# Performance work log

Measured on AMD Instinct MI355X. Metric: run time of the kernel, lower is better.

The kernel has to match this reference:

```python
import jax, jax.numpy as jnp
import numpy as np

QK_NOPE = 128
QK_ROPE = 64
V_DIM = 128
N_HEADS = 16
ROPE_BASE = 10000.0
RMS_EPS = 1e-6


def _rms_norm(x, w, eps=RMS_EPS):
    x = x.astype(jnp.float32)
    var = jnp.mean(x * x, axis=-1, keepdims=True)
    return w * x * jax.lax.rsqrt(var + eps)


def _rotate_half(x):
    x1, x2 = jnp.split(x, 2, axis=-1)
    return jnp.concatenate([-x2, x1], axis=-1)


def _rope_cos_sin(position_ids, dim=QK_ROPE, base=ROPE_BASE):
    # factor=1.0 YaRN collapses to plain RoPE with mscale=1
    inv_freq = 1.0 / (base ** (jnp.arange(0, dim, 2, dtype=jnp.float32) / dim))
    freqs = position_ids.astype(jnp.float32)[..., None] * inv_freq  # [B,S,dim/2]
    emb = jnp.concatenate([freqs, freqs], axis=-1)                  # [B,S,dim]
    return jnp.cos(emb), jnp.sin(emb)


def setup_inputs() -> dict:
    key = jax.random.key(0)
    ks = jax.random.split(key, 8)
    B, S, H = 1, 2048, 4096
    q_lora, kv_lora = 1536, 512
    q_head = QK_NOPE + QK_ROPE
    s = lambda k, shp, fan: jax.random.normal(k, shp, jnp.float32) * (fan ** -0.5)
    return {
        "hidden_states": jax.random.normal(ks[0], (B, S, H), jnp.float32),
        "position_ids": jnp.broadcast_to(jnp.arange(S, dtype=jnp.int64), (B, S)),
        "wq_a": s(ks[1], (q_lora, H), H),
        "q_a_norm_w": jnp.ones((q_lora,), jnp.float32),
        "wq_b": s(ks[2], (N_HEADS * q_head, q_lora), q_lora),
        "wkv_a": s(ks[3], (kv_lora + QK_ROPE, H), H),
        "kv_a_norm_w": jnp.ones((kv_lora,), jnp.float32),
        "wkv_b": s(ks[4], (N_HEADS * (QK_NOPE + V_DIM), kv_lora), kv_lora),
        "wo": s(ks[5], (H, N_HEADS * V_DIM), N_HEADS * V_DIM),
    }


def reference(hidden_states, position_ids, wq_a, q_a_norm_w, wq_b, wkv_a,
              kv_a_norm_w, wkv_b, wo):
    B, S, _ = hidden_states.shape
    kv_lora = kv_a_norm_w.shape[0]
    q_head = QK_NOPE + QK_ROPE
    softmax_scale = q_head ** -0.5  # mscale_all_dim=0 -> no yarn correction

    # Q low-rank path
    q_lat = _rms_norm(hidden_states @ wq_a.T, q_a_norm_w).astype(hidden_states.dtype)
    q = (q_lat @ wq_b.T).reshape(B, S, N_HEADS, q_head)
    q_nope, q_pe = q[..., :QK_NOPE], q[..., QK_NOPE:]

    # KV low-rank path
    kv = hidden_states @ wkv_a.T
    compressed_kv = _rms_norm(kv[..., :kv_lora], kv_a_norm_w).astype(hidden_states.dtype)
    k_pe = kv[..., kv_lora:].reshape(B, S, 1, QK_ROPE)

    cos, sin = _rope_cos_sin(position_ids)
    cos_h, sin_h = cos[:, :, None, :], sin[:, :, None, :]
    q_pe = q_pe * cos_h + _rotate_half(q_pe) * sin_h
    k_pe = k_pe * cos_h + _rotate_half(k_pe) * sin_h

    kv_exp = (compressed_kv @ wkv_b.T).reshape(B, S, N_HEADS, QK_NOPE + V_DIM)
    k_nope, v = kv_exp[..., :QK_NOPE], kv_exp[..., QK_NOPE:]

    qf = jnp.concatenate([q_nope, q_pe], axis=-1).astype(jnp.float32)   # [B,S,H,Dq]
    kf = jnp.concatenate([k_nope, jnp.broadcast_to(k_pe, (B, S, N_HEADS, QK_ROPE))],
                         axis=-1).astype(jnp.float32)
    vf = v.astype(jnp.float32)

    scores = jnp.einsum('bqhd,bkhd->bhqk', qf, kf) * softmax_scale
    causal = jnp.tril(jnp.ones((S, S), dtype=bool))
    scores = jnp.where(causal, scores, -jnp.inf)
    probs = jax.nn.softmax(scores, axis=-1)
    out = jnp.einsum('bhqk,bkhd->bqhd', probs, vf).astype(hidden_states.dtype)
    out = out.reshape(B, S, N_HEADS * V_DIM)
    return out @ wo.T
```

## Files before the change

kernel.cpp:

```cpp
#include <hip/hip_runtime.h>
#include <hip/hip_bf16.h>


typedef short bf16x8 __attribute__((ext_vector_type(8)));
typedef float f32x4  __attribute__((ext_vector_type(4)));

#if __has_builtin(__builtin_amdgcn_global_load_lds)
#define USE_GLL 1
#else
#define USE_GLL 0
#endif

__device__ __forceinline__ void stage16(const void* g, void* l) {
#if USE_GLL
    __builtin_amdgcn_global_load_lds(
        (__attribute__((address_space(1))) void*)(g),
        (__attribute__((address_space(3))) void*)(l), 16, 0, 0);
#else
    *(uint4*)l = *(const uint4*)g;
#endif
}

#define LOG2E 1.4426950408889634f

__device__ __forceinline__ short bf16_bits(float v) {
    union { __hip_bfloat16 h; short s; } u;
    u.h = __float2bfloat16(v);
    return u.s;
}

__global__ __launch_bounds__(256)
void cvt_bf16(const float* __restrict__ s, __hip_bfloat16* __restrict__ d, int nq) {
    int i = blockIdx.x * 256 + threadIdx.x;
    if (i >= nq) return;
    float4 v = ((const float4*)s)[i];
    union { uint2 u; __hip_bfloat16 h[4]; } r;
    r.h[0] = __float2bfloat16(v.x); r.h[1] = __float2bfloat16(v.y);
    r.h[2] = __float2bfloat16(v.z); r.h[3] = __float2bfloat16(v.w);
    ((uint2*)d)[i] = r.u;
}

__global__ __launch_bounds__(256)
void zero_f32(float* __restrict__ p, int n4) {
    int i = blockIdx.x * 256 + threadIdx.x;
    if (i < n4) ((float4*)p)[i] = float4{0.f, 0.f, 0.f, 0.f};
}

__global__ __launch_bounds__(256)
void zero_u4(uint4* __restrict__ p, int n) {
    int i = blockIdx.x * 256 + threadIdx.x;
    if (i < n) p[i] = make_uint4(0u, 0u, 0u, 0u);
}

__global__ __launch_bounds__(256)
void kpe_copy(const float* __restrict__ fused, float* __restrict__ kpe) {
    int i = blockIdx.x * 256 + threadIdx.x;
    int r = i >> 6, c = i & 63;
    kpe[i] = fused[(size_t)r * 2112 + 2048 + c];
}

template<int OUTMODE>
__global__ __launch_bounds__(256)
void gemm_lds(const __hip_bfloat16* __restrict__ A,
              const __hip_bfloat16* __restrict__ B,
              void* __restrict__ C,
              int K, int Cld, int Nlim, int ksteps) {
    __shared__ __align__(16) short As[128 * 64];
    __shared__ __align__(16) short Bs[128 * 64];

    const int tid  = threadIdx.x;
    const int lane = tid & 63;
    const int wave = tid >> 6;
    const int quad = lane >> 4;
    const int l16  = lane & 15;

    const int gx = gridDim.x, gy = gridDim.y;
    const int nwg = gx * gy * gridDim.z;
    const int f   = blockIdx.x + gx * (blockIdx.y + gy * blockIdx.z);
    const int qc  = nwg >> 3, rc = nwg & 7;
    const int xcd = f & 7, idx = f >> 3;
    const int neu = (xcd < rc ? xcd * (qc + 1) : rc * (qc + 1) + (xcd - rc) * qc) + idx;
    const int bx  = neu % gx;
    const int t1  = neu / gx;
    const int by  = t1 % gy;
    const int bz  = t1 / gy;

    const int m0 = by * 128;
    const int n0 = bx * 128;
    const int wm = (wave >> 1) * 64;
    const int wn = (wave & 1) * 64;
    const int kbeg = bz * ksteps * 64;

    const int lrow = lane >> 3;
    const int lchk = lane & 7;
    const int sb   = (lchk ^ lrow) * 16;

    f32x4 acc[4][4];
    #pragma unroll
    for (int i = 0; i < 4; i++)
        #pragma unroll
        for (int j = 0; j < 4; j++)
            acc[i][j] = f32x4{0.f, 0.f, 0.f, 0.f};

    const size_t str = (size_t)K * 2;
    const char* Ab = (const char*)A;
    const char* Bb = (const char*)B;

    for (int kk = 0; kk < ksteps; kk++) {
        if (kk) __syncthreads();
        const size_t koff = (size_t)(kbeg + kk * 64) * 2;
        #pragma unroll
        for (int t = 0; t < 4; t++) {
            const int row = wave * 32 + t * 8 + lrow;
            stage16(Ab + (size_t)(m0 + row) * str + koff + sb,
                    (char*)As + row * 128 + lchk * 16);
            stage16(Bb + (size_t)(n0 + row) * str + koff + sb,
                    (char*)Bs + row * 128 + lchk * 16);
        }
        __syncthreads();

        #pragma unroll
        for (int ks = 0; ks < 2; ks++) {
            const int ca = ((ks * 4 + quad) ^ (l16 & 7)) * 8;
            bf16x8 af[4], bfr[4];
            #pragma unroll
            for (int mi = 0; mi < 4; mi++)
                af[mi] = *(const bf16x8*)(&As[(wm + mi * 16 + l16) * 64 + ca]);
            #pragma unroll
            for (int ni = 0; ni < 4; ni++)
                bfr[ni] = *(const bf16x8*)(&Bs[(wn + ni * 16 + l16) * 64 + ca]);
            #pragma unroll
            for (int mi = 0; mi < 4; mi++)
                #pragma unroll
                for (int ni = 0; ni < 4; ni++)
                    acc[mi][ni] = __builtin_amdgcn_mfma_f32_16x16x32_bf16(
                        af[mi], bfr[ni], acc[mi][ni], 0, 0, 0);
        }
    }

    #pragma unroll
    for (int mi = 0; mi < 4; mi++)
        #pragma unroll
        for (int ni = 0; ni < 4; ni++) {
            const int col = n0 + wn + ni * 16 + l16;
            if (col >= Nlim) continue;
            #pragma unroll
            for (int r = 0; r < 4; r++) {
                const int row = m0 + wm + mi * 16 + quad * 4 + r;
                const float v = acc[mi][ni][r];
                if (OUTMODE == 0)
                    ((__hip_bfloat16*)C)[(size_t)row * Cld + col] = __float2bfloat16(v);
                else if (OUTMODE == 1)
                    ((float*)C)[(size_t)row * Cld + col] = v;
                else
                    atomicAdd(&((float*)C)[(size_t)row * Cld + col], v);
            }
        }
}

__global__ __launch_bounds__(256)
void rmsnorm_k(const float* __restrict__ X, const float* __restrict__ w,
               __hip_bfloat16* __restrict__ Y, int W, int sx, int sy) {
    int row = blockIdx.x;
    const float* x = X + (size_t)row * sx;
    float ss = 0.f;
    for (int i = threadIdx.x; i < W; i += 256) { float v = x[i]; ss += v * v; }
    for (int off = 32; off; off >>= 1) ss += __shfl_down(ss, off);
    __shared__ float red[4];
    int lane = threadIdx.x & 63, wv = threadIdx.x >> 6;
    if (lane == 0) red[wv] = ss;
    __syncthreads();
    float tot = red[0] + red[1] + red[2] + red[3];
    float inv = rsqrtf(tot / (float)W + 1e-6f);
    for (int i = threadIdx.x; i < W; i += 256) {
        float v = x[i] * inv * w[i];
        Y[(size_t)row * sy + i] = __float2bfloat16(v);
    }
}

__global__ __launch_bounds__(256)
void rope_assemble(__hip_bfloat16* __restrict__ q,
                   const __hip_bfloat16* __restrict__ kvexp,
                   const float* __restrict__ kpe_in,
                   __hip_bfloat16* __restrict__ kfT) {
    int s = blockIdx.x;
    int tid = threadIdx.x;
    __shared__ float cs[32], sn[32];
    __shared__ __hip_bfloat16 kpe[64];
    if (tid < 32) {
        float inv = expf(-(float)tid * (logf(10000.0f) / 32.0f));
        float ang = (float)s * inv;
        cs[tid] = cosf(ang);
        sn[tid] = sinf(ang);
    }
    __syncthreads();
    if (tid < 32) {
        float x1 = kpe_in[(size_t)s * 64 + tid];
        float x2 = kpe_in[(size_t)s * 64 + 32 + tid];
        kpe[tid]      = __float2bfloat16(x1 * cs[tid] - x2 * sn[tid]);
        kpe[tid + 32] = __float2bfloat16(x2 * cs[tid] + x1 * sn[tid]);
    }
    for (int p = tid; p < 512; p += 256) {
        int h = p >> 5, j = p & 31;
        size_t base = (size_t)s * 3072 + h * 192 + 128;
        float x1 = __bfloat162float(q[base + j]);
        float x2 = __bfloat162float(q[base + j + 32]);
        q[base + j]      = __float2bfloat16(x1 * cs[j] - x2 * sn[j]);
        q[base + j + 32] = __float2bfloat16(x2 * cs[j] + x1 * sn[j]);
    }
    __syncthreads();
    for (int i = tid; i < 16 * 192; i += 256) {
        int h = i / 192, d = i % 192;
        __hip_bfloat16 v = (d < 128) ? kvexp[(size_t)s * 4096 + h * 256 + d]
                                     : kpe[d - 128];
        kfT[((size_t)(h * 24 + (d >> 3)) * 2048 + s) * 8 + (d & 7)] = v;
    }
}

__global__ __launch_bounds__(256)
void transpose_v(const __hip_bfloat16* __restrict__ kvexp,
                 __hip_bfloat16* __restrict__ vT2) {
    __shared__ short t[64 * 72];
    int s0 = blockIdx.x * 64, d0 = blockIdx.y * 64, h = blockIdx.z;
    int c = threadIdx.x & 63;
    int r4 = threadIdx.x >> 6;
    for (int i = 0; i < 16; i++) {
        int r = r4 * 16 + i;
        t[r * 72 + c] = *(const short*)&kvexp[(size_t)(s0 + r) * 4096 + h * 256 + 128 + d0 + c];
    }
    __syncthreads();
    for (int it = 0; it < 2; it++) {
        int scl = it * 4 + (threadIdx.x >> 6);
        int d   = threadIdx.x & 63;
        union { uint4 u; short sh[8]; } pk;
        #pragma unroll
        for (int e = 0; e < 8; e++) pk.sh[e] = t[(scl * 8 + e) * 72 + d];
        size_t cell = ((size_t)h * 256 + blockIdx.x * 8 + scl) * 128 + d0 + d;
        ((uint4*)vT2)[cell] = pk.u;
    }
}

__global__ __launch_bounds__(256, 3)
void attn_kernel(const __hip_bfloat16* __restrict__ qb,
                 const __hip_bfloat16* __restrict__ kfT,
                 const __hip_bfloat16* __restrict__ vT2,
                 __hip_bfloat16* __restrict__ out) {
    const int b   = blockIdx.x;
    const int p   = b & 255;
    const int hi  = b >> 8;
    const int h   = p >> 4;
    const int j4  = p & 15;
    const int qt  = hi ? (31 - j4) : j4;
    const int q0  = qt * 64;
    const int tid  = threadIdx.x;
    const int wave = tid >> 6;
    const int lane = tid & 63;
    const int quad = lane >> 4;
    const int l16  = lane & 15;

    __shared__ __align__(16) short Ks2[24 * 64 * 8];
    __shared__ __align__(16) short Vs2[ 8 * 128 * 8];
    __shared__ __align__(16) short Ps2[ 8 * 64 * 8];

    const float scale = 0.07216878364870322f;

    bf16x8 qfr[6];
    {
        int row = q0 + wave * 16 + l16;
        const __hip_bfloat16* qrow = qb + ((size_t)row * 16 + h) * 192;
        for (int ks = 0; ks < 6; ks++) {
            union { bf16x8 v; __hip_bfloat16 h8[8]; } u;
            u.v = *(const bf16x8*)(qrow + ks * 32 + quad * 8);
            #pragma unroll
            for (int e = 0; e < 8; e++)
                u.h8[e] = __float2bfloat16(__bfloat162float(u.h8[e]) * scale);
            qfr[ks] = u.v;
        }
    }

    f32x4 o_acc[8];
    #pragma unroll
    for (int i = 0; i < 8; i++) o_acc[i] = f32x4{0.f, 0.f, 0.f, 0.f};
    float m_i[4], l_i[4];
    #pragma unroll
    for (int r = 0; r < 4; r++) { m_i[r] = -__builtin_inff(); l_i[r] = 0.f; }

    const char* kfb = (const char*)kfT;
    const char* vtb = (const char*)vT2;

    for (int kt = 0; kt <= qt; kt++) {
        if (kt) __syncthreads();
        #pragma unroll
        for (int j = 0; j < 6; j++) {
            int c = wave * 6 + j;
            stage16(kfb + (((size_t)(h * 24 + c) * 2048) + kt * 64 + lane) * 16,
                    (char*)Ks2 + (c * 64 + lane) * 16);
        }
        #pragma unroll
        for (int j = 0; j < 4; j++) {
            int c  = wave * 2 + (j >> 1);
            int hd = j & 1;
            stage16(vtb + (((size_t)(h * 256 + kt * 8 + c) * 128) + hd * 64 + lane) * 16,
                    (char*)Vs2 + (c * 128 + hd * 64 + lane) * 16);
        }
        __syncthreads();

        f32x4 sc[4];
        #pragma unroll
        for (int n = 0; n < 4; n++) sc[n] = f32x4{0.f, 0.f, 0.f, 0.f};
        #pragma unroll
        for (int ks = 0; ks < 6; ks++)
            #pragma unroll
            for (int n = 0; n < 4; n++) {
                bf16x8 kb = *(const bf16x8*)(&Ks2[((ks * 4 + quad) * 64 + n * 16 + l16) * 8]);
                sc[n] = __builtin_amdgcn_mfma_f32_16x16x32_bf16(qfr[ks], kb, sc[n], 0, 0, 0);
            }

        const bool last = (kt == qt);
        float tmax[4], rsum[4], alpha[4];
        #pragma unroll
        for (int r = 0; r < 4; r++) tmax[r] = -__builtin_inff();
        #pragma unroll
        for (int n = 0; n < 4; n++)
            #pragma unroll
            for (int r = 0; r < 4; r++) {
                float v = sc[n][r];
                if (last && (kt * 64 + n * 16 + l16) > (q0 + wave * 16 + quad * 4 + r))
                    v = -__builtin_inff();
                sc[n][r] = v;
                tmax[r] = fmaxf(tmax[r], v);
            }
        #pragma unroll
        for (int r = 0; r < 4; r++)
            #pragma unroll
            for (int off = 1; off < 16; off <<= 1)
                tmax[r] = fmaxf(tmax[r], __shfl_xor(tmax[r], off));
        #pragma unroll
        for (int r = 0; r < 4; r++) {
            float mn = fmaxf(m_i[r], tmax[r]);
            alpha[r] = exp2f((m_i[r] - mn) * LOG2E);
            m_i[r] = mn;
            rsum[r] = 0.f;
        }
        #pragma unroll
        for (int n = 0; n < 4; n++)
            #pragma unroll
            for (int r = 0; r < 4; r++) {
                float p2 = exp2f((sc[n][r] - m_i[r]) * LOG2E);
                sc[n][r] = p2;
                rsum[r] += p2;
            }
        #pragma unroll
        for (int r = 0; r < 4; r++) {
            #pragma unroll
            for (int off = 1; off < 16; off <<= 1)
                rsum[r] += __shfl_xor(rsum[r], off);
            l_i[r] = l_i[r] * alpha[r] + rsum[r];
        }
        #pragma unroll
        for (int n = 0; n < 4; n++)
            #pragma unroll
            for (int r = 0; r < 4; r++)
                Ps2[((n * 2 + (l16 >> 3)) * 64 + wave * 16 + quad * 4 + r) * 8 + (l16 & 7)] =
                    bf16_bits(sc[n][r]);
        #pragma unroll
        for (int d = 0; d < 8; d++)
            #pragma unroll
            for (int r = 0; r < 4; r++)
                o_acc[d][r] *= alpha[r];
        #pragma unroll
        for (int ks2 = 0; ks2 < 2; ks2++) {
            bf16x8 pa = *(const bf16x8*)(&Ps2[((ks2 * 4 + quad) * 64 + wave * 16 + l16) * 8]);
            #pragma unroll
            for (int dg = 0; dg < 8; dg++) {
                bf16x8 vb = *(const bf16x8*)(&Vs2[((ks2 * 4 + quad) * 128 + dg * 16 + l16) * 8]);
                o_acc[dg] = __builtin_amdgcn_mfma_f32_16x16x32_bf16(pa, vb, o_acc[dg], 0, 0, 0);
            }
        }
    }

    #pragma unroll
    for (int dg = 0; dg < 8; dg++)
        #pragma unroll
        for (int r = 0; r < 4; r++) {
            int row = q0 + wave * 16 + quad * 4 + r;
            float v = o_acc[dg][r] / l_i[r];
            out[((size_t)row * 16 + h) * 128 + dg * 16 + l16] = __float2bfloat16(v);
        }
}

extern "C" void kernel_launch(void* const* d_in, const int* in_sizes, int n_in,
                              void* d_out, int out_size, void* d_ws, size_t ws_size,
                              hipStream_t stream) {
    const float* hidden = (const float*)d_in[0];
    const float* wq_a   = (const float*)d_in[2];
    const float* q_a_w  = (const float*)d_in[3];
    const float* wq_b   = (const float*)d_in[4];
    const float* wkv_a  = (const float*)d_in[5];
    const float* kv_a_w = (const float*)d_in[6];
    const float* wkv_b  = (const float*)d_in[7];
    const float* wo     = (const float*)d_in[8];
    float* out = (float*)d_out;

    char* ws = (char*)d_ws;
    __hip_bfloat16* hiddenB = (__hip_bfloat16*)(ws + 0);
    __hip_bfloat16* wq_bB   = (__hip_bfloat16*)(ws + 0);
    __hip_bfloat16* kfT     = (__hip_bfloat16*)(ws + 0);
    __hip_bfloat16* W0      = (__hip_bfloat16*)(ws + 16777216);
    __hip_bfloat16* kv_exp  = (__hip_bfloat16*)(ws + 16777216);
    __hip_bfloat16* attn_o  = (__hip_bfloat16*)(ws + 16777216);
    float*          fused   = (float*)(ws + 34603008);
    __hip_bfloat16* qb      = (__hip_bfloat16*)(ws + 34603008);
    __hip_bfloat16* woB     = (__hip_bfloat16*)(ws + 34603008);
    __hip_bfloat16* wkv_bB  = (__hip_bfloat16*)(ws + 47185920);
    float*          kpe     = (float*)(ws + 51904512);
    __hip_bfloat16* q_lat   = (__hip_bfloat16*)(ws + 52428800);
    __hip_bfloat16* vT2     = (__hip_bfloat16*)(ws + 52428800);
    __hip_bfloat16* ckv     = (__hip_bfloat16*)(ws + 58720256);

    dim3 blk(256);
    cvt_bf16<<<8192, blk, 0, stream>>>(hidden, hiddenB, 2097152);
    cvt_bf16<<<6144, blk, 0, stream>>>(wq_a,  W0,               1572864);
    cvt_bf16<<<2304, blk, 0, stream>>>(wkv_a, W0 + 1536 * 4096,  589824);
    zero_u4<<<128, blk, 0, stream>>>((uint4*)(W0 + 2112 * 4096), 32768);
    zero_f32<<<4224, blk, 0, stream>>>(fused, 1081344);
    gemm_lds<2><<<dim3(17, 16, 4), blk, 0, stream>>>(hiddenB, W0, fused, 4096, 2112, 2112, 16);
    kpe_copy<<<512, blk, 0, stream>>>(fused, kpe);
    rmsnorm_k<<<2048, blk, 0, stream>>>(fused,        q_a_w,  q_lat, 1536, 2112, 1536);
    rmsnorm_k<<<2048, blk, 0, stream>>>(fused + 1536, kv_a_w, ckv,    512, 2112,  512);
    cvt_bf16<<<4608, blk, 0, stream>>>(wq_b,  wq_bB,  1179648);
    cvt_bf16<<<2048, blk, 0, stream>>>(wkv_b, wkv_bB,  524288);
    gemm_lds<0><<<dim3(24, 16), blk, 0, stream>>>(q_lat, wq_bB,  qb,     1536, 3072, 3072, 24);
    gemm_lds<0><<<dim3(32, 16), blk, 0, stream>>>(ckv,   wkv_bB, kv_exp,  512, 4096, 4096,  8);
    rope_assemble<<<2048, blk, 0, stream>>>(qb, kv_exp, kpe, kfT);
    transpose_v<<<dim3(32, 2, 16), blk, 0, stream>>>(kv_exp, vT2);
    attn_kernel<<<dim3(512), blk, 0, stream>>>(qb, kfT, vT2, attn_o);
    cvt_bf16<<<8192, blk, 0, stream>>>(wo, woB, 2097152);
    gemm_lds<1><<<dim3(32, 16), blk, 0, stream>>>(attn_o, woB, out, 2048, 4096, 4096, 32);
}
```

Before: 458.9 us.

## Split long causal attention tiles across two blocks and merge partial results

The attention grid grows from 512 to 768 blocks. Each of the 256 long query tiles (qt 16..31) has its key range split into two halves, and each half is computed by its own block, which writes an unnormalized fp32 output plus its row max and row sum to workspace. A new merge kernel then combines the two partials with a log-sum-exp rescale. This shortens the longest blocks and evens out the causal load imbalance, at the cost of an extra launch and fp32 partial traffic through scattered workspace regions.

```diff
diff --git a/kernel.cpp b/kernel.cpp
--- a/kernel.cpp
+++ b/kernel.cpp
@@ -27,6 +27,13 @@
     union { __hip_bfloat16 h; short s; } u;
     u.h = __float2bfloat16(v);
     return u.s;
+}
+
+__device__ __forceinline__ const float* po_base(const float* b0, const float* b1,
+                                                const float* b2, int pid) {
+    if (pid < 288) return b0 + (size_t)pid * 8192;
+    if (pid < 448) return b1 + (size_t)(pid - 288) * 8192;
+    return b2 + (size_t)(pid - 448) * 8192;
 }
 
 __global__ __launch_bounds__(256)
@@ -244,14 +251,25 @@
 void attn_kernel(const __hip_bfloat16* __restrict__ qb,
                  const __hip_bfloat16* __restrict__ kfT,
                  const __hip_bfloat16* __restrict__ vT2,
-                 __hip_bfloat16* __restrict__ out) {
-    const int b   = blockIdx.x;
-    const int p   = b & 255;
-    const int hi  = b >> 8;
-    const int h   = p >> 4;
-    const int j4  = p & 15;
-    const int qt  = hi ? (31 - j4) : j4;
-    const int q0  = qt * 64;
+                 __hip_bfloat16* __restrict__ out,
+                 float* __restrict__ po0, float* __restrict__ po1,
+                 float* __restrict__ po2,
+                 float* __restrict__ pm, float* __restrict__ pl) {
+    const int b = blockIdx.x;
+    int h, qt, ktbeg, ktend, pid;
+    if (b < 256) {
+        h = b >> 4; qt = b & 15;
+        ktbeg = 0; ktend = qt + 1; pid = -1;
+    } else {
+        const int idx  = (b - 256) & 255;
+        const int part = (b - 256) >> 8;
+        h = idx >> 4; qt = 31 - (idx & 15);
+        const int n0 = (qt + 2) >> 1;
+        ktbeg = part ? n0 : 0;
+        ktend = part ? qt + 1 : n0;
+        pid = part * 256 + idx;
+    }
+    const int q0   = qt * 64;
     const int tid  = threadIdx.x;
     const int wave = tid >> 6;
     const int lane = tid & 63;
@@ -288,8 +306,8 @@
     const char* kfb = (const char*)kfT;
     const char* vtb = (const char*)vT2;
 
-    for (int kt = 0; kt <= qt; kt++) {
-        if (kt) __syncthreads();
+    for (int kt = ktbeg; kt < ktend; kt++) {
+        if (kt != ktbeg) __syncthreads();
         #pragma unroll
         for (int j = 0; j < 6; j++) {
             int c = wave * 6 + j;
@@ -379,14 +397,68 @@
         }
     }
 
+    if (pid < 0) {
+        #pragma unroll
+        for (int dg = 0; dg < 8; dg++)
+            #pragma unroll
+            for (int r = 0; r < 4; r++) {
+                int row = q0 + wave * 16 + quad * 4 + r;
+                float v = o_acc[dg][r] / l_i[r];
+                out[((size_t)row * 16 + h) * 128 + dg * 16 + l16] = __float2bfloat16(v);
+            }
+    } else {
+        float* pob = const_cast<float*>(po_base(po0, po1, po2, pid));
+        #pragma unroll
+        for (int dg = 0; dg < 8; dg++)
+            #pragma unroll
+            for (int r = 0; r < 4; r++) {
+                int lr = wave * 16 + quad * 4 + r;
+                pob[(size_t)lr * 128 + dg * 16 + l16] = o_acc[dg][r];
+            }
+        if (l16 == 0) {
+            #pragma unroll
+            for (int r = 0; r < 4; r++) {
+                int lr = wave * 16 + quad * 4 + r;
+                pm[pid * 64 + lr] = m_i[r];
+                pl[pid * 64 + lr] = l_i[r];
+            }
+        }
+    }
+}
+
+__global__ __launch_bounds__(256)
+void attn_merge(const float* __restrict__ po0, const float* __restrict__ po1,
+                const float* __restrict__ po2,
+                const float* __restrict__ pm, const float* __restrict__ pl,
+                __hip_bfloat16* __restrict__ out) {
+    const int idx = blockIdx.x;
+    const int h  = idx >> 4;
+    const int qt = 31 - (idx & 15);
+    const int q0 = qt * 64;
+    const int t   = threadIdx.x;
+    const int row = t >> 2;
+    const int c0  = (t & 3) << 5;
+    const int pid0 = idx, pid1 = 256 + idx;
+    const float m0 = pm[pid0 * 64 + row], m1 = pm[pid1 * 64 + row];
+    const float l0 = pl[pid0 * 64 + row], l1 = pl[pid1 * 64 + row];
+    const float M  = fmaxf(m0, m1);
+    const float e0 = exp2f((m0 - M) * LOG2E);
+    const float e1 = exp2f((m1 - M) * LOG2E);
+    const float inv = 1.f / (e0 * l0 + e1 * l1);
+    const float* p0 = po_base(po0, po1, po2, pid0) + (size_t)row * 128 + c0;
+    const float* p1 = po_base(po0, po1, po2, pid1) + (size_t)row * 128 + c0;
+    __hip_bfloat16* o = out + ((size_t)(q0 + row) * 16 + h) * 128 + c0;
     #pragma unroll
-    for (int dg = 0; dg < 8; dg++)
-        #pragma unroll
-        for (int r = 0; r < 4; r++) {
-            int row = q0 + wave * 16 + quad * 4 + r;
-            float v = o_acc[dg][r] / l_i[r];
-            out[((size_t)row * 16 + h) * 128 + dg * 16 + l16] = __float2bfloat16(v);
-        }
+    for (int c = 0; c < 32; c += 4) {
+        float4 a = *(const float4*)(p0 + c);
+        float4 bb = *(const float4*)(p1 + c);
+        union { uint2 u; __hip_bfloat16 hh[4]; } w;
+        w.hh[0] = __float2bfloat16((e0 * a.x + e1 * bb.x) * inv);
+        w.hh[1] = __float2bfloat16((e0 * a.y + e1 * bb.y) * inv);
+        w.hh[2] = __float2bfloat16((e0 * a.z + e1 * bb.z) * inv);
+        w.hh[3] = __float2bfloat16((e0 * a.w + e1 * bb.w) * inv);
+        *(uint2*)(o + c) = w.u;
+    }
 }
 
 extern "C" void kernel_launch(void* const* d_in, const int* in_sizes, int n_in,
@@ -417,6 +489,11 @@
     __hip_bfloat16* q_lat   = (__hip_bfloat16*)(ws + 52428800);
     __hip_bfloat16* vT2     = (__hip_bfloat16*)(ws + 52428800);
     __hip_bfloat16* ckv     = (__hip_bfloat16*)(ws + 58720256);
+    float* po0 = (float*)(ws + 25165824);
+    float* po1 = (float*)(ws + 47185920);
+    float* po2 = (float*)(ws + 12582912);
+    float* pm  = (float*)(ws + 14680064);
+    float* pl  = (float*)(ws + 14811136);
 
     dim3 blk(256);
     cvt_bf16<<<8192, blk, 0, stream>>>(hidden, hiddenB, 2097152);
@@ -434,7 +511,8 @@
     gemm_lds<0><<<dim3(32, 16), blk, 0, stream>>>(ckv,   wkv_bB, kv_exp,  512, 4096, 4096,  8);
     rope_assemble<<<2048, blk, 0, stream>>>(qb, kv_exp, kpe, kfT);
     transpose_v<<<dim3(32, 2, 16), blk, 0, stream>>>(kv_exp, vT2);
-    attn_kernel<<<dim3(512), blk, 0, stream>>>(qb, kfT, vT2, attn_o);
+    attn_kernel<<<dim3(768), blk, 0, stream>>>(qb, kfT, vT2, attn_o, po0, po1, po2, pm, pl);
+    attn_merge<<<dim3(256), blk, 0, stream>>>(po0, po1, po2, pm, pl, attn_o);
     cvt_bf16<<<8192, blk, 0, stream>>>(wo, woB, 2097152);
     gemm_lds<1><<<dim3(32, 16), blk, 0, stream>>>(attn_o, woB, out, 2048, 4096, 4096, 32);
 }
```

Result: no change. 453.4 us (-1.2%).
